# Performance work log

Measured on AMD Instinct MI355X. Metric: run time of the kernel, lower is better.

## Reference

```python
import jax, jax.numpy as jnp
import numpy as np

EMB = 768
N_HEADS = 12
HEAD_DIM = EMB // N_HEADS


def setup_inputs() -> dict:
    key = jax.random.key(0)
    k_x, k_w1, k_b1, k_w2, k_b2 = jax.random.split(key, 5)
    B, T = 8, 1024
    s = 0.02
    return {
        "x": jax.random.normal(k_x, (B, T, EMB), dtype=jnp.float32),
        "w_attn": jax.random.normal(k_w1, (EMB, 3 * EMB), dtype=jnp.float32) * s,
        "b_attn": jax.random.normal(k_b1, (3 * EMB,), dtype=jnp.float32) * s,
        "w_proj": jax.random.normal(k_w2, (EMB, EMB), dtype=jnp.float32) * s,
        "b_proj": jax.random.normal(k_b2, (EMB,), dtype=jnp.float32) * s,
    }


def reference(x, w_attn, b_attn, w_proj, b_proj):
    B, T, C = x.shape
    qkv = x @ w_attn + b_attn                       # [B,T,3C]
    q, k, v = jnp.split(qkv, 3, axis=2)
    # [B,T,C] -> [B,H,T,D]
    q = q.reshape(B, T, N_HEADS, HEAD_DIM).transpose(0, 2, 1, 3)
    k = k.reshape(B, T, N_HEADS, HEAD_DIM).transpose(0, 2, 1, 3)
    v = v.reshape(B, T, N_HEADS, HEAD_DIM).transpose(0, 2, 1, 3)
    scale = HEAD_DIM ** -0.5
    att = jnp.einsum("bhqd,bhkd->bhqk", q, k) * scale  # [B,H,T,T]
    causal = jnp.tril(jnp.ones((T, T), dtype=bool))
    att = jnp.where(causal, att, -jnp.inf)
    att = jax.nn.softmax(att, axis=-1)
    out = jnp.einsum("bhqk,bhkd->bhqd", att, v)        # [B,H,T,D]
    out = out.transpose(0, 2, 1, 3).reshape(B, T, C)
    return out @ w_proj + b_proj
```

## Files before the change

kernel.cpp:

```cpp
#include <hip/hip_runtime.h>
#include <hip/hip_bf16.h>
#include <math.h>

#define BATCH 8
#define SEQ   1024
#define EMB   768
#define NH    12
#define HD    64
#define QKVW  (3 * EMB)
#define VOFF  (2 * EMB)

typedef short short8   __attribute__((ext_vector_type(8)));
typedef float floatx4  __attribute__((ext_vector_type(4)));

__device__ __forceinline__ short f2bf(float f) {
    union { float f; unsigned u; } v; v.f = f;
    unsigned r = (v.u + 0x7fffu + ((v.u >> 16) & 1u)) >> 16;
    return (short)r;
}

__device__ __forceinline__ void async_load16(const void* g, void* l) {
    __builtin_amdgcn_global_load_lds(
        (const __attribute__((address_space(1))) unsigned int*)g,
        (__attribute__((address_space(3))) unsigned int*)l, 16, 0, 0);
}

__global__ __launch_bounds__(256) void cvt_bf16(
    const float* __restrict__ in, short* __restrict__ out, int n8)
{
    const int i = blockIdx.x * 256 + threadIdx.x;
    if (i >= n8) return;
    const float4 a = ((const float4*)in)[2 * i];
    const float4 b = ((const float4*)in)[2 * i + 1];
    short8 s;
    s[0] = f2bf(a.x); s[1] = f2bf(a.y); s[2] = f2bf(a.z); s[3] = f2bf(a.w);
    s[4] = f2bf(b.x); s[5] = f2bf(b.y); s[6] = f2bf(b.z); s[7] = f2bf(b.w);
    ((short8*)out)[i] = s;
}

__global__ __launch_bounds__(256) void transpose_to_bf16(
    const float* __restrict__ in, short* __restrict__ outT, int R, int C)
{
    __shared__ float t[32][33];
    const int c0 = blockIdx.x * 32, r0 = blockIdx.y * 32;
    const int lx = threadIdx.x & 31, ly = threadIdx.x >> 5;
    #pragma unroll
    for (int i = 0; i < 32; i += 8)
        t[ly + i][lx] = in[(size_t)(r0 + ly + i) * C + c0 + lx];
    __syncthreads();
    #pragma unroll
    for (int i = 0; i < 32; i += 8)
        outT[(size_t)(c0 + ly + i) * R + r0 + lx] = f2bf(t[lx][ly + i]);
}

#define NT12 (EMB / 64)

#define BAR()    do { asm volatile("" ::: "memory"); __builtin_amdgcn_s_barrier(); \
                      asm volatile("" ::: "memory"); } while (0)
#define LGKM0()  asm volatile("s_waitcnt lgkmcnt(0)" ::: "memory")
#define VMC0()   asm volatile("s_waitcnt vmcnt(0)" ::: "memory")
#define VMC4()   asm volatile("s_waitcnt vmcnt(4)" ::: "memory")
#define VMC8()   asm volatile("s_waitcnt vmcnt(8)" ::: "memory")
#define SCHED0() __builtin_amdgcn_sched_barrier(0)
#define PRIO1()  __builtin_amdgcn_s_setprio(1)
#define PRIO0()  __builtin_amdgcn_s_setprio(0)


#define LDA(bf_, r_, q_) (*(const short8*)&As[bf_][(r_) * 64 + ((((q_)) ^ ((r_) & 7)) << 3)])
#define LDB(bf_, r_, q_) (*(const short8*)&Bs[bf_][(r_) * 64 + ((((q_)) ^ ((r_) & 7)) << 3)])

#define MMA_T(IB, JB)                                                        \
    _Pragma("unroll")                                                        \
    for (int kk = 0; kk < 2; ++kk)                                           \
        _Pragma("unroll")                                                    \
        for (int mi = 0; mi < 4; ++mi)                                       \
            _Pragma("unroll")                                                \
            for (int nj = 0; nj < 2; ++nj)                                   \
                acc[(IB) + mi][(JB) + nj] =                                  \
                    __builtin_amdgcn_mfma_f32_16x16x32_bf16(                 \
                        b[(JB) + nj][kk], a[mi][kk],                         \
                        acc[(IB) + mi][(JB) + nj], 0, 0, 0);

#define MMA_D(IB, JB)                                                        \
    _Pragma("unroll")                                                        \
    for (int kk = 0; kk < 2; ++kk)                                           \
        _Pragma("unroll")                                                    \
        for (int mi = 0; mi < 4; ++mi)                                       \
            _Pragma("unroll")                                                \
            for (int nj = 0; nj < 2; ++nj)                                   \
                acc[(IB) + mi][(JB) + nj] =                                  \
                    __builtin_amdgcn_mfma_f32_16x16x32_bf16(                 \
                        a[mi][kk], b[(JB) + nj][kk],                         \
                        acc[(IB) + mi][(JB) + nj], 0, 0, 0);

#define KLOOP(MM)                                                            \
    for (int kt = 0; kt < NT12; ++kt) {                                      \
        const int buf = kt & 1;                                              \
                    \
        _Pragma("unroll")                                                    \
        for (int mi = 0; mi < 4; ++mi)                                       \
            _Pragma("unroll")                                                \
            for (int kk = 0; kk < 2; ++kk)                                   \
                a[mi][kk] = LDA(buf, ar0 + mi * 16, quad + kk * 4);          \
        _Pragma("unroll")                                                    \
        for (int nj = 0; nj < 2; ++nj)                                       \
            _Pragma("unroll")                                                \
            for (int kk = 0; kk < 2; ++kk)                                   \
                b[nj][kk] = LDB(buf, br0 + nj * 16, quad + kk * 4);          \
        BAR(); LGKM0(); SCHED0();                                            \
        PRIO1(); MM(0, 0); PRIO0();                                          \
        BAR();                                                               \
                                    \
        _Pragma("unroll")                                                    \
        for (int nj = 2; nj < 4; ++nj)                                       \
            _Pragma("unroll")                                                \
            for (int kk = 0; kk < 2; ++kk)                                   \
                b[nj][kk] = LDB(buf, br0 + nj * 16, quad + kk * 4);          \
        BAR(); LGKM0(); SCHED0();                                            \
        PRIO1(); MM(0, 2); PRIO0();                                          \
        BAR();                                                               \
             \
        _Pragma("unroll")                                                    \
        for (int mi = 0; mi < 4; ++mi)                                       \
            _Pragma("unroll")                                                \
            for (int kk = 0; kk < 2; ++kk)                                   \
                a[mi][kk] = LDA(buf, ar0 + 64 + mi * 16, quad + kk * 4);     \
        stage_half(kt + 2, 2); stage_half(kt + 2, 3);                        \
        BAR(); LGKM0(); SCHED0();                                            \
        PRIO1(); MM(4, 2); PRIO0();                                          \
        BAR();                                                               \
                           \
        stage_half(kt + 2, 0); stage_half(kt + 2, 1);                        \
        SCHED0();                                                            \
        PRIO1(); MM(4, 0); PRIO0();                                          \
        if (kt + 2 < NT12) { VMC8(); } else { VMC0(); }                      \
        BAR();                                                               \
    }

__global__ __launch_bounds__(512, 2) void gemm_qkv_256(
    const short* __restrict__ A, const short* __restrict__ Bt,
    const float* __restrict__ bias, short* __restrict__ qkvb,
    short* __restrict__ vt)
{
    __shared__ __align__(16) short As[2][256 * 64];
    __shared__ __align__(16) short Bs[2][256 * 64];

    const int tid  = threadIdx.x;
    const int wave = tid >> 6;
    const int lane = tid & 63;
    const int ln15 = lane & 15;
    const int quad = lane >> 4;
    const int wm   = wave >> 2;
    const int wn   = wave & 3;

    const int orig = blockIdx.x;
    const int wg   = (orig & 7) * 36 + (orig >> 3);
    const int bx   = wg % (QKVW / 256);
    const int by   = wg / (QKVW / 256);
    const int row0 = by * 256;
    const int col0 = bx * 256;
    const bool vpath = (col0 >= VOFF);

    const short* Ag = A  + (size_t)row0 * EMB;
    const short* Bg = Bt + (size_t)col0 * EMB;

    auto stage_half = [&](int t, int h) {
        if (t >= NT12) return;
        const int buf   = t & 1;
        const int k0    = t * 64;
        const int rbase = (h & 1) * 128;
        short* lb       = (h < 2) ? &As[buf][rbase * 64] : &Bs[buf][rbase * 64];
        const short* gb = (h < 2) ? Ag : Bg;
        #pragma unroll
        for (int p = 0; p < 2; ++p) {
            const int id  = p * 512 + tid;
            const int row = rbase + (id >> 3);
            const int c   = (id & 7) ^ (row & 7);
            async_load16(gb + (size_t)row * EMB + k0 + c * 8, lb + (size_t)id * 8);
        }
    };

    floatx4 acc[8][4];
    #pragma unroll
    for (int i = 0; i < 8; ++i)
        #pragma unroll
        for (int j = 0; j < 4; ++j) acc[i][j] = (floatx4){0.f, 0.f, 0.f, 0.f};

    short8 a[4][2];
    short8 b[4][2];

    #pragma unroll
    for (int h = 0; h < 4; ++h) stage_half(0, h);
    #pragma unroll
    for (int h = 0; h < 4; ++h) stage_half(1, h);
    VMC8();
    BAR();

    const int ar0 = wm * 128 + ln15;
    const int br0 = wn * 64 + ln15;

    if (vpath) { KLOOP(MMA_D) } else { KLOOP(MMA_T) }

    if (!vpath) {
        #pragma unroll
        for (int j = 0; j < 4; ++j) {
            const float4 b4 = *(const float4*)&bias[col0 + wn * 64 + j * 16 + quad * 4];
            #pragma unroll
            for (int i = 0; i < 8; ++i) {
                const int r = row0 + wm * 128 + i * 16 + ln15;
                const int c = col0 + wn * 64 + j * 16 + quad * 4;
                union { short s[4]; unsigned long long u; } pk;
                pk.s[0] = f2bf(acc[i][j][0] + b4.x);
                pk.s[1] = f2bf(acc[i][j][1] + b4.y);
                pk.s[2] = f2bf(acc[i][j][2] + b4.z);
                pk.s[3] = f2bf(acc[i][j][3] + b4.w);
                *(unsigned long long*)&qkvb[(size_t)r * QKVW + c] = pk.u;
            }
        }
    } else {
        #pragma unroll
        for (int j = 0; j < 4; ++j) {
            const int c  = col0 + wn * 64 + j * 16 + ln15;
            const float bv = bias[c];
            const int c2 = c - VOFF;
            #pragma unroll
            for (int i = 0; i < 8; ++i) {
                const int r = row0 + wm * 128 + i * 16 + quad * 4;
                union { short s[4]; unsigned long long u; } pk;
                #pragma unroll
                for (int reg = 0; reg < 4; ++reg)
                    pk.s[reg] = f2bf(acc[i][j][reg] + bv);
                *(unsigned long long*)&vt[(size_t)(r >> 10) * (EMB * SEQ) +
                                          (size_t)c2 * SEQ + (r & 1023)] = pk.u;
            }
        }
    }
}


#define LDA8(bf_, r_, q_) (*(const short8*)&As[bf_][(r_) * 64 + ((((q_)) ^ ((r_) & 7)) << 3)])
#define LDB8(bf_, r_, q_) (*(const short8*)&Bs[bf_][(r_) * 64 + ((((q_)) ^ ((r_) & 7)) << 3)])

#define MMA_T2(JB)                                                           \
    _Pragma("unroll")                                                        \
    for (int kk = 0; kk < 2; ++kk)                                           \
        _Pragma("unroll")                                                    \
        for (int mi = 0; mi < 4; ++mi)                                       \
            _Pragma("unroll")                                                \
            for (int nj = 0; nj < 2; ++nj)                                   \
                acc[mi][(JB) + nj] =                                         \
                    __builtin_amdgcn_mfma_f32_16x16x32_bf16(                 \
                        b[(JB) + nj][kk], a[mi][kk],                         \
                        acc[mi][(JB) + nj], 0, 0, 0);

#define KLOOP2(MM)                                                           \
    for (int kt = 0; kt < NT12; ++kt) {                                      \
        const int buf = kt & 1;                                              \
                 \
        _Pragma("unroll")                                                    \
        for (int mi = 0; mi < 4; ++mi)                                       \
            _Pragma("unroll")                                                \
            for (int kk = 0; kk < 2; ++kk)                                   \
                a[mi][kk] = LDA8(buf, ar0 + mi * 16, quad + kk * 4);         \
        _Pragma("unroll")                                                    \
        for (int nj = 0; nj < 2; ++nj)                                       \
            _Pragma("unroll")                                                \
            for (int kk = 0; kk < 2; ++kk)                                   \
                b[nj][kk] = LDB8(buf, br0 + nj * 16, quad + kk * 4);         \
        if (kt + 1 < NT12) stage_B(kt + 1);                                  \
        BAR(); LGKM0(); SCHED0();                                            \
        PRIO1(); MM(0); PRIO0();                                             \
        BAR();                                                               \
                     \
        _Pragma("unroll")                                                    \
        for (int nj = 2; nj < 4; ++nj)                                       \
            _Pragma("unroll")                                                \
            for (int kk = 0; kk < 2; ++kk)                                   \
                b[nj][kk] = LDB8(buf, br0 + nj * 16, quad + kk * 4);         \
        if (kt + 2 < NT12) stage_A(kt + 2);                                  \
        BAR(); LGKM0(); SCHED0();                                            \
        PRIO1(); MM(2); PRIO0();                                             \
        if (kt + 2 < NT12) {                                                 \
            if (wuni < 4) { VMC4(); } else { VMC0(); }                       \
        } else if (kt + 1 < NT12) { VMC0(); }                                \
        BAR();                                                               \
    }

__global__ __launch_bounds__(384, 3) void gemm_proj(
    const short* __restrict__ A, const short* __restrict__ Bt,
    const float* __restrict__ bias, float* __restrict__ Cout,
    int N, int nbx)
{
    __shared__ __align__(16) short As[2][128 * 64];
    __shared__ __align__(16) short Bs[2][192 * 64];

    const int tid  = threadIdx.x;
    const int wave = tid >> 6;
    const int lane = tid & 63;
    const int ln15 = lane & 15;
    const int quad = lane >> 4;
    const int wm   = wave / 3;
    const int wn   = wave % 3;
    const int wuni = __builtin_amdgcn_readfirstlane(wave);

    const int orig = blockIdx.x;
    const int wg   = (orig & 7) * (8 * nbx) + (orig >> 3);
    const int bx   = wg % nbx;
    const int by   = wg / nbx;
    const int row0 = by * 128;
    const int col0 = bx * 192;

    const short* Ag = A  + (size_t)row0 * EMB;
    const short* Bg = Bt + (size_t)col0 * EMB;

    auto stage_A = [&](int t) {
        if (wave >= 4) return;
        const int buf = t & 1;
        #pragma unroll
        for (int p = 0; p < 4; ++p) {
            const int id  = (wave * 4 + p) * 64 + lane;
            const int row = id >> 3;
            const int c   = (id & 7) ^ (row & 7);
            async_load16(Ag + (size_t)row * EMB + t * 64 + c * 8, &As[buf][id * 8]);
        }
    };
    auto stage_B = [&](int t) {
        const int buf = t & 1;
        #pragma unroll
        for (int p = 0; p < 4; ++p) {
            const int id  = (wave * 4 + p) * 64 + lane;
            const int row = id >> 3;
            const int c   = (id & 7) ^ (row & 7);
            async_load16(Bg + (size_t)row * EMB + t * 64 + c * 8, &Bs[buf][id * 8]);
        }
    };

    floatx4 acc[4][4];
    #pragma unroll
    for (int i = 0; i < 4; ++i)
        #pragma unroll
        for (int j = 0; j < 4; ++j) acc[i][j] = (floatx4){0.f, 0.f, 0.f, 0.f};

    short8 a[4][2];
    short8 b[4][2];

    stage_A(0); stage_B(0); stage_A(1);
    if (wuni < 4) { VMC4(); } else { VMC0(); }
    BAR();

    const int ar0 = wm * 64 + ln15;
    const int br0 = wn * 64 + ln15;

    KLOOP2(MMA_T2)

    const int wr = wm * 64, wc = wn * 64;
    float4 b4[4];
    #pragma unroll
    for (int j = 0; j < 4; ++j)
        b4[j] = *(const float4*)&bias[col0 + wc + j * 16 + quad * 4];
    #pragma unroll
    for (int i = 0; i < 4; ++i) {
        const int r = row0 + wr + i * 16 + ln15;
        #pragma unroll
        for (int j = 0; j < 4; ++j) {
            const int c = col0 + wc + j * 16 + quad * 4;
            float4 v;
            v.x = acc[i][j][0] + b4[j].x;
            v.y = acc[i][j][1] + b4[j].y;
            v.z = acc[i][j][2] + b4[j].z;
            v.w = acc[i][j][3] + b4[j].w;
            *(float4*)&Cout[(size_t)r * N + c] = v;
        }
    }
}

#define LDK 72

__global__ __launch_bounds__(256) void attn_mfma(
    const short* __restrict__ qkv, const short* __restrict__ vt,
    short* __restrict__ out)
{
    __shared__ __align__(16) short Ks[64 * LDK];
    __shared__ __align__(16) short Vt[64 * LDK];
    __shared__ __align__(16) short Ps[4 * 16 * LDK];

    const int tid  = threadIdx.x;
    const int wave = tid >> 6;
    const int lane = tid & 63;
    const int ln15 = lane & 15;
    const int quad = lane >> 4;

    const int qc = 15 - (int)(blockIdx.x / (BATCH * NH));
    const int bh = blockIdx.x % (BATCH * NH);
    const int h  = bh % NH;
    const int b  = bh / NH;

    const int q0w = qc * 64 + wave * 16;

    const short* qkv_b = qkv + (size_t)b * SEQ * QKVW + h * HD;
    const short* Kg  = qkv_b + EMB;
    const short* Vtg = vt + ((size_t)b * EMB + h * HD) * SEQ;

    short8 qf[2];
    {
        const short* qrow = qkv_b + (size_t)(q0w + ln15) * QKVW;
        qf[0] = *(const short8*)(qrow + quad * 8);
        qf[1] = *(const short8*)(qrow + quad * 8 + 32);
    }

    floatx4 o[4];
    #pragma unroll
    for (int i = 0; i < 4; ++i) o[i] = (floatx4){0.f, 0.f, 0.f, 0.f};
    float lp[4] = {0.f, 0.f, 0.f, 0.f};

    const int rr = tid >> 3;
    const int c8 = (tid & 7) * 8;

    for (int kt = 0; kt <= qc; ++kt) {
        #pragma unroll
        for (int p = 0; p < 2; ++p) {
            const int r2 = rr + p * 32;
            *(uint4*)&Ks[r2 * LDK + c8] =
                *(const uint4*)(Kg + (size_t)(kt * 64 + r2) * QKVW + c8);
            *(uint4*)&Vt[r2 * LDK + c8] =
                *(const uint4*)(Vtg + (size_t)r2 * SEQ + kt * 64 + c8);
        }
        __syncthreads();

        floatx4 s[4];
        #pragma unroll
        for (int i = 0; i < 4; ++i) s[i] = (floatx4){0.f, 0.f, 0.f, 0.f};
        #pragma unroll
        for (int st = 0; st < 2; ++st)
            #pragma unroll
            for (int sub = 0; sub < 4; ++sub) {
                const short8 kf = *(const short8*)&Ks[(ln15 + sub * 16) * LDK + quad * 8 + st * 32];
                s[sub] = __builtin_amdgcn_mfma_f32_16x16x32_bf16(qf[st], kf, s[sub], 0, 0, 0);
            }

        const bool diag = (kt == qc);
        #pragma unroll
        for (int sub = 0; sub < 4; ++sub)
            #pragma unroll
            for (int reg = 0; reg < 4; ++reg) {
                float pv = __expf(s[sub][reg] * 0.125f);
                if (diag && (ln15 + sub * 16 > wave * 16 + quad * 4 + reg)) pv = 0.f;
                s[sub][reg] = pv;
            }
        #pragma unroll
        for (int reg = 0; reg < 4; ++reg)
            lp[reg] += (s[0][reg] + s[1][reg]) + (s[2][reg] + s[3][reg]);

        short* Pw = &Ps[wave * 16 * LDK];
        #pragma unroll
        for (int sub = 0; sub < 4; ++sub)
            #pragma unroll
            for (int reg = 0; reg < 4; ++reg) {
                const int qr   = quad * 4 + reg;
                const int kr8  = sub * 2 + (ln15 >> 3);
                const int slot = (kr8 + 5 * quad + reg) & 7;
                Pw[qr * LDK + slot * 8 + (ln15 & 7)] = f2bf(s[sub][reg]);
            }

        short8 pf[2];
        #pragma unroll
        for (int st = 0; st < 2; ++st) {
            const int slot = ((quad + 4 * st) + 5 * (ln15 >> 2) + (ln15 & 3)) & 7;
            pf[st] = *(const short8*)&Pw[ln15 * LDK + slot * 8];
        }

        #pragma unroll
        for (int st = 0; st < 2; ++st)
            #pragma unroll
            for (int sub = 0; sub < 4; ++sub) {
                const short8 vf = *(const short8*)&Vt[(ln15 + sub * 16) * LDK + quad * 8 + st * 32];
                o[sub] = __builtin_amdgcn_mfma_f32_16x16x32_bf16(pf[st], vf, o[sub], 0, 0, 0);
            }

        __syncthreads();
    }

    #pragma unroll
    for (int reg = 0; reg < 4; ++reg) {
        float t = lp[reg];
        #pragma unroll
        for (int off = 1; off <= 8; off <<= 1)
            t += __shfl_xor(t, off, 64);
        const float inv = 1.0f / t;
        const size_t row = (size_t)(b * SEQ + q0w + quad * 4 + reg) * EMB + h * HD;
        #pragma unroll
        for (int sub = 0; sub < 4; ++sub)
            out[row + ln15 + sub * 16] = f2bf(o[sub][reg] * inv);
    }
}

extern "C" void kernel_launch(void* const* d_in, const int* in_sizes, int n_in,
                              void* d_out, int out_size, void* d_ws, size_t ws_size,
                              hipStream_t stream)
{
    const float* x      = (const float*)d_in[0];
    const float* w_attn = (const float*)d_in[1];
    const float* b_attn = (const float*)d_in[2];
    const float* w_proj = (const float*)d_in[3];
    const float* b_proj = (const float*)d_in[4];
    float* out = (float*)d_out;

    const int M = BATCH * SEQ;

    short* xb    = (short*)d_ws;
    short* waT   = xb    + (size_t)M * EMB;
    short* wpT   = waT   + (size_t)QKVW * EMB;
    short* qkvb  = wpT   + (size_t)EMB * EMB;
    short* vtb   = qkvb  + (size_t)M * QKVW;
    short* attnb = vtb   + (size_t)BATCH * EMB * SEQ;

    dim3 blk(256);

    cvt_bf16<<<dim3((M * EMB) / 8 / 256), blk, 0, stream>>>(x, xb, (M * EMB) / 8);
    transpose_to_bf16<<<dim3(QKVW / 32, EMB / 32), blk, 0, stream>>>(w_attn, waT, EMB, QKVW);
    transpose_to_bf16<<<dim3(EMB / 32, EMB / 32), blk, 0, stream>>>(w_proj, wpT, EMB, EMB);

    gemm_qkv_256<<<dim3((QKVW / 256) * (M / 256)), dim3(512), 0, stream>>>(
        xb, waT, b_attn, qkvb, vtb);

    attn_mfma<<<dim3(16 * BATCH * NH), blk, 0, stream>>>(qkvb, vtb, attnb);

    gemm_proj<<<dim3((M / 128) * (EMB / 192)), dim3(384), 0, stream>>>(
        attnb, wpT, b_proj, out, EMB, EMB / 192);
}
```

Baseline: 212.7 us.

## Shrink QKV GEMM to 128x128 tiles with 4 waves and split A/B staging

Replaces the 256x256 QKV projection GEMM (512 threads, 8 waves) with a 128x128-tile version using 256 threads and 4 waves, giving 1152 workgroups instead of 288. The prefetch pipeline is restructured so B is staged one k-step ahead and A two steps ahead, with matching vmcnt waits. The aim is better load balance across the CUs, a better-filled final wave and lower LDS use per block. In exchange, each tile reuses data less, so global and L2 traffic per FLOP goes up.

```diff
diff --git a/kernel.cpp b/kernel.cpp
--- a/kernel.cpp
+++ b/kernel.cpp
@@ -60,11 +60,9 @@
 #define LGKM0()  asm volatile("s_waitcnt lgkmcnt(0)" ::: "memory")
 #define VMC0()   asm volatile("s_waitcnt vmcnt(0)" ::: "memory")
 #define VMC4()   asm volatile("s_waitcnt vmcnt(4)" ::: "memory")
-#define VMC8()   asm volatile("s_waitcnt vmcnt(8)" ::: "memory")
 #define SCHED0() __builtin_amdgcn_sched_barrier(0)
 #define PRIO1()  __builtin_amdgcn_s_setprio(1)
 #define PRIO0()  __builtin_amdgcn_s_setprio(0)
-
 
 #define LDA(bf_, r_, q_) (*(const short8*)&As[bf_][(r_) * 64 + ((((q_)) ^ ((r_) & 7)) << 3)])
 #define LDB(bf_, r_, q_) (*(const short8*)&Bs[bf_][(r_) * 64 + ((((q_)) ^ ((r_) & 7)) << 3)])
@@ -93,10 +91,10 @@
                         a[mi][kk], b[(JB) + nj][kk],                         \
                         acc[(IB) + mi][(JB) + nj], 0, 0, 0);
 
-#define KLOOP(MM)                                                            \
+#define KLOOPQ(MM)                                                           \
     for (int kt = 0; kt < NT12; ++kt) {                                      \
         const int buf = kt & 1;                                              \
-                    \
+            \
         _Pragma("unroll")                                                    \
         for (int mi = 0; mi < 4; ++mi)                                       \
             _Pragma("unroll")                                                \
@@ -107,108 +105,98 @@
             _Pragma("unroll")                                                \
             for (int kk = 0; kk < 2; ++kk)                                   \
                 b[nj][kk] = LDB(buf, br0 + nj * 16, quad + kk * 4);          \
+        if (kt + 1 < NT12) stage_B(kt + 1);                                  \
         BAR(); LGKM0(); SCHED0();                                            \
         PRIO1(); MM(0, 0); PRIO0();                                          \
         BAR();                                                               \
-                                    \
+               \
         _Pragma("unroll")                                                    \
         for (int nj = 2; nj < 4; ++nj)                                       \
             _Pragma("unroll")                                                \
             for (int kk = 0; kk < 2; ++kk)                                   \
                 b[nj][kk] = LDB(buf, br0 + nj * 16, quad + kk * 4);          \
+        if (kt + 2 < NT12) stage_A(kt + 2);                                  \
         BAR(); LGKM0(); SCHED0();                                            \
         PRIO1(); MM(0, 2); PRIO0();                                          \
+        if (kt + 2 < NT12) { VMC4(); } else if (kt + 1 < NT12) { VMC0(); }   \
         BAR();                                                               \
-             \
-        _Pragma("unroll")                                                    \
-        for (int mi = 0; mi < 4; ++mi)                                       \
-            _Pragma("unroll")                                                \
-            for (int kk = 0; kk < 2; ++kk)                                   \
-                a[mi][kk] = LDA(buf, ar0 + 64 + mi * 16, quad + kk * 4);     \
-        stage_half(kt + 2, 2); stage_half(kt + 2, 3);                        \
-        BAR(); LGKM0(); SCHED0();                                            \
-        PRIO1(); MM(4, 2); PRIO0();                                          \
-        BAR();                                                               \
-                           \
-        stage_half(kt + 2, 0); stage_half(kt + 2, 1);                        \
-        SCHED0();                                                            \
-        PRIO1(); MM(4, 0); PRIO0();                                          \
-        if (kt + 2 < NT12) { VMC8(); } else { VMC0(); }                      \
-        BAR();                                                               \
-    }
-
-__global__ __launch_bounds__(512, 2) void gemm_qkv_256(
+    }
+
+__global__ __launch_bounds__(256, 2) void gemm_qkv_128(
     const short* __restrict__ A, const short* __restrict__ Bt,
     const float* __restrict__ bias, short* __restrict__ qkvb,
     short* __restrict__ vt)
 {
-    __shared__ __align__(16) short As[2][256 * 64];
-    __shared__ __align__(16) short Bs[2][256 * 64];
+    __shared__ __align__(16) short As[2][128 * 64];
+    __shared__ __align__(16) short Bs[2][128 * 64];
 
     const int tid  = threadIdx.x;
     const int wave = tid >> 6;
     const int lane = tid & 63;
     const int ln15 = lane & 15;
     const int quad = lane >> 4;
-    const int wm   = wave >> 2;
-    const int wn   = wave & 3;
+    const int wm   = wave >> 1;
+    const int wn   = wave & 1;
 
     const int orig = blockIdx.x;
-    const int wg   = (orig & 7) * 36 + (orig >> 3);
-    const int bx   = wg % (QKVW / 256);
-    const int by   = wg / (QKVW / 256);
-    const int row0 = by * 256;
-    const int col0 = bx * 256;
+    const int wg   = (orig & 7) * 144 + (orig >> 3);
+    const int bx   = wg % (QKVW / 128);
+    const int by   = wg / (QKVW / 128);
+    const int row0 = by * 128;
+    const int col0 = bx * 128;
     const bool vpath = (col0 >= VOFF);
 
     const short* Ag = A  + (size_t)row0 * EMB;
     const short* Bg = Bt + (size_t)col0 * EMB;
 
-    auto stage_half = [&](int t, int h) {
-        if (t >= NT12) return;
-        const int buf   = t & 1;
-        const int k0    = t * 64;
-        const int rbase = (h & 1) * 128;
-        short* lb       = (h < 2) ? &As[buf][rbase * 64] : &Bs[buf][rbase * 64];
-        const short* gb = (h < 2) ? Ag : Bg;
-        #pragma unroll
-        for (int p = 0; p < 2; ++p) {
-            const int id  = p * 512 + tid;
-            const int row = rbase + (id >> 3);
+    auto stage_A = [&](int t) {
+        const int buf = t & 1;
+        #pragma unroll
+        for (int p = 0; p < 4; ++p) {
+            const int id  = p * 256 + tid;
+            const int row = id >> 3;
             const int c   = (id & 7) ^ (row & 7);
-            async_load16(gb + (size_t)row * EMB + k0 + c * 8, lb + (size_t)id * 8);
+            async_load16(Ag + (size_t)row * EMB + t * 64 + c * 8, &As[buf][id * 8]);
         }
     };
-
-    floatx4 acc[8][4];
-    #pragma unroll
-    for (int i = 0; i < 8; ++i)
+    auto stage_B = [&](int t) {
+        const int buf = t & 1;
+        #pragma unroll
+        for (int p = 0; p < 4; ++p) {
+            const int id  = p * 256 + tid;
+            const int row = id >> 3;
+            const int c   = (id & 7) ^ (row & 7);
+            async_load16(Bg + (size_t)row * EMB + t * 64 + c * 8, &Bs[buf][id * 8]);
+        }
+    };
+
+    floatx4 acc[4][4];
+    #pragma unroll
+    for (int i = 0; i < 4; ++i)
         #pragma unroll
         for (int j = 0; j < 4; ++j) acc[i][j] = (floatx4){0.f, 0.f, 0.f, 0.f};
 
     short8 a[4][2];
     short8 b[4][2];
 
-    #pragma unroll
-    for (int h = 0; h < 4; ++h) stage_half(0, h);
-    #pragma unroll
-    for (int h = 0; h < 4; ++h) stage_half(1, h);
-    VMC8();
+    stage_A(0); stage_B(0); stage_A(1);
+    VMC4();
     BAR();
 
-    const int ar0 = wm * 128 + ln15;
+    const int ar0 = wm * 64 + ln15;
     const int br0 = wn * 64 + ln15;
 
-    if (vpath) { KLOOP(MMA_D) } else { KLOOP(MMA_T) }
-
+    if (vpath) { KLOOPQ(MMA_D) } else { KLOOPQ(MMA_T) }
+
+    const int wr = wm * 64, wc = wn * 64;
     if (!vpath) {
         #pragma unroll
         for (int j = 0; j < 4; ++j) {
-            const float4 b4 = *(const float4*)&bias[col0 + wn * 64 + j * 16 + quad * 4];
+            const float4 b4 = *(const float4*)&bias[col0 + wc + j * 16 + quad * 4];
             #pragma unroll
-            for (int i = 0; i < 8; ++i) {
-                const int r = row0 + wm * 128 + i * 16 + ln15;
-                const int c = col0 + wn * 64 + j * 16 + quad * 4;
+            for (int i = 0; i < 4; ++i) {
+                const int r = row0 + wr + i * 16 + ln15;
+                const int c = col0 + wc + j * 16 + quad * 4;
                 union { short s[4]; unsigned long long u; } pk;
                 pk.s[0] = f2bf(acc[i][j][0] + b4.x);
                 pk.s[1] = f2bf(acc[i][j][1] + b4.y);
@@ -220,12 +208,12 @@
     } else {
         #pragma unroll
         for (int j = 0; j < 4; ++j) {
-            const int c  = col0 + wn * 64 + j * 16 + ln15;
+            const int c  = col0 + wc + j * 16 + ln15;
             const float bv = bias[c];
             const int c2 = c - VOFF;
             #pragma unroll
-            for (int i = 0; i < 8; ++i) {
-                const int r = row0 + wm * 128 + i * 16 + quad * 4;
+            for (int i = 0; i < 4; ++i) {
+                const int r = row0 + wr + i * 16 + quad * 4;
                 union { short s[4]; unsigned long long u; } pk;
                 #pragma unroll
                 for (int reg = 0; reg < 4; ++reg)
@@ -520,7 +508,7 @@
     transpose_to_bf16<<<dim3(QKVW / 32, EMB / 32), blk, 0, stream>>>(w_attn, waT, EMB, QKVW);
     transpose_to_bf16<<<dim3(EMB / 32, EMB / 32), blk, 0, stream>>>(w_proj, wpT, EMB, EMB);
 
-    gemm_qkv_256<<<dim3((QKVW / 256) * (M / 256)), dim3(512), 0, stream>>>(
+    gemm_qkv_128<<<dim3((M / 128) * (QKVW / 128)), blk, 0, stream>>>(
         xb, waT, b_attn, qkvb, vtb);
 
     attn_mfma<<<dim3(16 * BATCH * NH), blk, 0, stream>>>(qkvb, vtb, attnb);
```

Result: faster. 200.7 us (-5.7%).
